# Kernel tuning notes

Measured on AMD Instinct MI355X. Metric: run time of the kernel, lower is better.

Reference implementation:

```python
import jax, jax.numpy as jnp
import numpy as np

N_N = 100000
N_E = 1600000
IN_DIM = 128
OUT_DIM = 128


def setup_inputs() -> dict:
    key = jax.random.key(0)
    k1, k2, k3, k4 = jax.random.split(key, 4)
    feats_n = jax.random.normal(k1, (N_N, IN_DIM), dtype=jnp.float32)
    # hs: guarantee every node appears at least once as a row (head) so degree > 0,
    # matching well-posed inputs for D**(-1/2) in the original module.
    hs = jnp.concatenate([
        jnp.arange(N_N, dtype=jnp.int64),
        jax.random.randint(k2, (N_E - N_N,), 0, N_N, dtype=jnp.int64),
    ])
    ts = jax.random.randint(k3, (N_E,), 0, N_N, dtype=jnp.int64)
    edges = jnp.stack([hs, ts], axis=0)  # [2, N_e]
    # Linear weight: normal(0,1) scaled by 1/sqrt(out_dim), no bias.
    weight = jax.random.normal(k4, (OUT_DIM, IN_DIM), dtype=jnp.float32) / np.sqrt(OUT_DIM)
    return {"feats_n": feats_n, "edges": edges, "weight": weight}


def reference(feats_n, edges, weight):
    hs, ts = edges[0], edges[1]
    n = feats_n.shape[0]
    # Degree = row-sum of adjacency (rows indexed by hs)
    deg = jax.ops.segment_sum(jnp.ones_like(hs, dtype=feats_n.dtype), hs, num_segments=n)
    sqrt_d_inv = deg ** (-0.5)  # [N_n]
    scaled = sqrt_d_inv[:, None] * feats_n  # [N_n, d]
    # SpMM: out[h] = sum over edges (h, t) of scaled[t]
    agg = jax.ops.segment_sum(scaled[ts], hs, num_segments=n)  # [N_n, d]
    msg = sqrt_d_inv[:, None] * agg
    out = msg @ weight.T  # Linear, no bias
    return jax.nn.relu(out)
```

## Files before the change

kernel.cpp:

```cpp
#include <hip/hip_runtime.h>

#define IN_DIM 128
#define CAP 64
#define NODE_SHIFT 8
#define BIN_NODES 256
#define NB_MAX 512
#define BCAP 5120
#define BINCAP_E 10240
#define CHUNK 4096
#define SMEM_BYTES 32768

typedef __attribute__((ext_vector_type(8))) short bf16x8;
typedef __attribute__((ext_vector_type(4))) float f32x4;
typedef __attribute__((ext_vector_type(2))) float f32x2;

struct PtLds { int hist[NB_MAX]; int base[NB_MAX]; unsigned int sp[CHUNK]; };
struct BsLds { unsigned int sp[BCAP]; int lcur[BIN_NODES]; int sbase[BIN_NODES];
               int wsum[4]; };

__device__ __forceinline__ unsigned short f2bf(float f) {
    unsigned int u = __float_as_uint(f);
    u += 0x7FFFu + ((u >> 16) & 1u);
    return (unsigned short)(u >> 16);
}

__device__ __forceinline__ void dev_partition(char* smem, int c, const int* __restrict__ edges,
                                              int n_e, int nbins,
                                              unsigned int* __restrict__ pairs,
                                              int* __restrict__ bincur) {
    PtLds* pt = (PtLds*)smem;
    int tid = threadIdx.x;
    int e0 = c * CHUNK;
    int nloc = n_e - e0;
    if (nloc > CHUNK) nloc = CHUNK;
    int nloc4 = nloc >> 2;
    const int* hsrc = edges + e0;
    const int* tsrc = edges + n_e + e0;
    for (int i = tid; i < nbins; i += 256) pt->hist[i] = 0;
    __syncthreads();
    for (int j = tid; j < nloc4; j += 256) {
        int4 hv = ((const int4*)hsrc)[j];
        int4 tv = ((const int4*)tsrc)[j];
        pt->sp[4 * j + 0] = ((unsigned int)(hv.x & 255) << 17) | (unsigned int)tv.x;
        pt->sp[4 * j + 1] = ((unsigned int)(hv.y & 255) << 17) | (unsigned int)tv.y;
        pt->sp[4 * j + 2] = ((unsigned int)(hv.z & 255) << 17) | (unsigned int)tv.z;
        pt->sp[4 * j + 3] = ((unsigned int)(hv.w & 255) << 17) | (unsigned int)tv.w;
        atomicAdd(&pt->hist[hv.x >> NODE_SHIFT], 1);
        atomicAdd(&pt->hist[hv.y >> NODE_SHIFT], 1);
        atomicAdd(&pt->hist[hv.z >> NODE_SHIFT], 1);
        atomicAdd(&pt->hist[hv.w >> NODE_SHIFT], 1);
    }
    for (int i = (nloc4 << 2) + tid; i < nloc; i += 256) {
        int h = hsrc[i];
        pt->sp[i] = ((unsigned int)(h & 255) << 17) | (unsigned int)tsrc[i];
        atomicAdd(&pt->hist[h >> NODE_SHIFT], 1);
    }
    __syncthreads();
    for (int b = tid; b < nbins; b += 256) {
        int cc = pt->hist[b];
        pt->base[b] = cc ? atomicAdd(&bincur[b], cc) : 0;
        pt->hist[b] = 0;
    }
    __syncthreads();
    for (int j = tid; j < nloc4; j += 256) {
        int4 hv = ((const int4*)hsrc)[j];
        int bi[4] = {hv.x >> NODE_SHIFT, hv.y >> NODE_SHIFT,
                     hv.z >> NODE_SHIFT, hv.w >> NODE_SHIFT};
        #pragma unroll
        for (int k = 0; k < 4; ++k) {
            int b = bi[k];
            int pos = atomicAdd(&pt->hist[b], 1);
            int g = pt->base[b] + pos;
            if (g < BCAP) pairs[(size_t)b * BCAP + g] = pt->sp[4 * j + k];
        }
    }
    for (int i = (nloc4 << 2) + tid; i < nloc; i += 256) {
        int b = hsrc[i] >> NODE_SHIFT;
        int pos = atomicAdd(&pt->hist[b], 1);
        int g = pt->base[b] + pos;
        if (g < BCAP) pairs[(size_t)b * BCAP + g] = pt->sp[i];
    }
    __syncthreads();
}

__device__ __forceinline__ void dev_binscatter(char* smem, int b,
                                               const unsigned int* __restrict__ pairs,
                                               const int* __restrict__ bincur,
                                               int* __restrict__ bucket,
                                               int2* __restrict__ rowinfo,
                                               float* __restrict__ rsd, int n_n) {
    BsLds* bs = (BsLds*)smem;
    int tid = threadIdx.x;
    bs->lcur[tid] = 0;
    __syncthreads();
    int n = bincur[b];
    if (n > BCAP) n = BCAP;
    const unsigned int* pp = pairs + (size_t)b * BCAP;
    for (int i = tid; i < n; i += 256) {
        unsigned int p = pp[i];
        bs->sp[i] = p;
        atomicAdd(&bs->lcur[p >> 17], 1);
    }
    __syncthreads();
    int draw = bs->lcur[tid];
    int dcap = draw < CAP ? draw : CAP;
    int v = (dcap + 15) & ~15;
    int lane = tid & 63, w = tid >> 6;
    int x = v;
    #pragma unroll
    for (int off = 1; off < 64; off <<= 1) {
        int y = __shfl_up(x, off);
        if (lane >= off) x += y;
    }
    if (lane == 63) bs->wsum[w] = x;
    __syncthreads();
    int wo = 0;
    for (int k = 0; k < w; ++k) wo += bs->wsum[k];
    int mybase = wo + x - v;
    bs->sbase[tid] = mybase;
    bs->lcur[tid] = 0;
    __syncthreads();
    int gbase = b * BINCAP_E;
    for (int i = tid; i < n; i += 256) {
        unsigned int p = bs->sp[i];
        int li = p >> 17;
        int t = p & 0x1FFFF;
        int pos = atomicAdd(&bs->lcur[li], 1);
        if (pos < CAP) {
            int idx = bs->sbase[li] + pos;
            if (idx < BINCAP_E) bucket[gbase + idx] = t;
        }
    }
    __syncthreads();
    int h = (b << NODE_SHIFT) + tid;
    if (h < n_n) {
        for (int s = dcap; s < v; ++s) {
            int idx = mybase + s;
            if (idx < BINCAP_E) bucket[gbase + idx] = n_n;
        }
        rowinfo[h] = make_int2(gbase + mybase, dcap);
        rsd[h] = draw > 0 ? rsqrtf((float)draw) : 0.0f;
    } else if (h == n_n) {
        rsd[n_n] = 0.0f;
    }
    __syncthreads();
}

__device__ __forceinline__ void dev_wconv(char* smem, const float* __restrict__ W) {
    bf16x8* wl = (bf16x8*)smem;
    int tid = threadIdx.x;
    #pragma unroll
    for (int k = 0; k < 8; ++k) {
        int gi = tid + k * 256;
        int n = gi >> 4, g = gi & 15;
        const float* wp = W + n * IN_DIM + g * 8;
        float4 a = *(const float4*)wp;
        float4 b2 = *(const float4*)(wp + 4);
        bf16x8 v;
        v[0] = (short)f2bf(a.x); v[1] = (short)f2bf(a.y);
        v[2] = (short)f2bf(a.z); v[3] = (short)f2bf(a.w);
        v[4] = (short)f2bf(b2.x); v[5] = (short)f2bf(b2.y);
        v[6] = (short)f2bf(b2.z); v[7] = (short)f2bf(b2.w);
        wl[n * 16 + (g ^ (n & 7))] = v;
    }
    __syncthreads();
}

__device__ __forceinline__ void dev_gemm(char* smem, int mb, const float* __restrict__ X,
                                         unsigned short* __restrict__ Y2, int M) {
    const bf16x8* wl = (const bf16x8*)smem;
    int tid = threadIdx.x;
    int slab = mb * 4 + (tid >> 6);
    int m0 = slab * 16;
    if (m0 >= M) return;
    int l = tid & 63;
    int lm = l & 15, lk = l >> 4;
    int row = m0 + lm;
    int rowc = row < M ? row : M - 1;
    bf16x8 xf[4];
    const float* xbase = X + (size_t)rowc * IN_DIM + lk * 8;
    #pragma unroll
    for (int ks = 0; ks < 4; ++ks) {
        float4 a = *(const float4*)(xbase + ks * 32);
        float4 b2 = *(const float4*)(xbase + ks * 32 + 4);
        bf16x8 v;
        v[0] = (short)f2bf(a.x); v[1] = (short)f2bf(a.y);
        v[2] = (short)f2bf(a.z); v[3] = (short)f2bf(a.w);
        v[4] = (short)f2bf(b2.x); v[5] = (short)f2bf(b2.y);
        v[6] = (short)f2bf(b2.z); v[7] = (short)f2bf(b2.w);
        xf[ks] = v;
    }
    #pragma unroll
    for (int nt = 0; nt < 8; ++nt) {
        f32x4 acc = {0.f, 0.f, 0.f, 0.f};
        #pragma unroll
        for (int ks = 0; ks < 4; ++ks) {
            int nn = nt * 16 + lm;
            int g = ks * 4 + lk;
            bf16x8 wf = wl[nn * 16 + (g ^ (nn & 7))];
            acc = __builtin_amdgcn_mfma_f32_16x16x32_bf16(wf, xf[ks], acc, 0, 0, 0);
        }
        if (row < M) {
            unsigned int lo = (unsigned int)f2bf(acc[0]) |
                              ((unsigned int)f2bf(acc[1]) << 16);
            unsigned int hi = (unsigned int)f2bf(acc[2]) |
                              ((unsigned int)f2bf(acc[3]) << 16);
            uint2* yp = (uint2*)(Y2 + (size_t)row * IN_DIM + nt * 16 + lk * 4);
            *yp = make_uint2(lo, hi);
        }
    }
}

__global__ __launch_bounds__(256, 4) void k_phaseA(const int* __restrict__ edges, int n_e,
                                                   int nbins, int npart, int mbA, int split,
                                                   unsigned int* __restrict__ pairs,
                                                   int* __restrict__ bincur,
                                                   const float* __restrict__ X,
                                                   const float* __restrict__ W,
                                                   unsigned short* __restrict__ Y2, int n_n) {
    extern __shared__ char smem[];
    int bid = blockIdx.x, NB = gridDim.x;
    if (bid < split) {
        for (int c = bid; c < npart; c += split)
            dev_partition(smem, c, edges, n_e, nbins, pairs, bincur);
    } else {
        dev_wconv(smem, W);
        for (int mb = bid - split; mb < mbA; mb += NB - split)
            dev_gemm(smem, mb, X, Y2, n_n);
    }
}

__global__ __launch_bounds__(256, 4) void k_phaseB(int nbins, int mbA, int nmf, int split,
                                                   const unsigned int* __restrict__ pairs,
                                                   const int* __restrict__ bincur,
                                                   int* __restrict__ bucket,
                                                   int2* __restrict__ rowinfo,
                                                   float* __restrict__ rsd,
                                                   const float* __restrict__ X,
                                                   const float* __restrict__ W,
                                                   unsigned short* __restrict__ Y2, int n_n) {
    extern __shared__ char smem[];
    int bid = blockIdx.x, NB = gridDim.x;
    if (bid < split) {
        for (int b = bid; b < nbins; b += split)
            dev_binscatter(smem, b, pairs, bincur, bucket, rowinfo, rsd, n_n);
    } else {
        dev_wconv(smem, W);
        for (int mb = mbA + (bid - split); mb < nmf; mb += NB - split)
            dev_gemm(smem, mb, X, Y2, n_n);
    }
}

__global__ __launch_bounds__(256) void k_agg(const uint4* __restrict__ Y4,
                                             const int* __restrict__ bucket,
                                             const int2* __restrict__ rowinfo,
                                             const float* __restrict__ rsd,
                                             float* __restrict__ out, int n_n) {
    int gw = (int)((blockIdx.x * 256u + threadIdx.x) >> 6);
    int lane = threadIdx.x & 63;
    if (gw >= n_n) return;
    int2 ri = rowinfo[gw];
    int d = ri.y;
    int nb = (d + 15) >> 4;
    const uint4* bk4 = (const uint4*)(bucket + ri.x);
    int grp = lane >> 4, a = lane & 15;
    f32x2 a0 = {0.f, 0.f}, a1 = {0.f, 0.f}, a2 = {0.f, 0.f}, a3 = {0.f, 0.f};

    uint4 tv = bk4[grp];
    for (int b = 0; b < nb; ++b) {
        int bn = (b + 1 < nb) ? b + 1 : b;
        uint4 tvn = bk4[bn * 4 + grp];
        float s0 = rsd[tv.x], s1 = rsd[tv.y], s2 = rsd[tv.z], s3 = rsd[tv.w];
        uint4 v0 = Y4[(size_t)tv.x * 16 + a];
        uint4 v1 = Y4[(size_t)tv.y * 16 + a];
        uint4 v2 = Y4[(size_t)tv.z * 16 + a];
        uint4 v3 = Y4[(size_t)tv.w * 16 + a];
        #define ACCUM(V, S)                                                   \
        {                                                                     \
            f32x2 sv; sv[0] = (S); sv[1] = (S);                               \
            f32x2 x;                                                          \
            x[0] = __uint_as_float((V).x << 16);                              \
            x[1] = __uint_as_float((V).x & 0xffff0000u);                      \
            asm("v_pk_fma_f32 %0, %1, %2, %0" : "+v"(a0) : "v"(x), "v"(sv));  \
            x[0] = __uint_as_float((V).y << 16);                              \
            x[1] = __uint_as_float((V).y & 0xffff0000u);                      \
            asm("v_pk_fma_f32 %0, %1, %2, %0" : "+v"(a1) : "v"(x), "v"(sv));  \
            x[0] = __uint_as_float((V).z << 16);                              \
            x[1] = __uint_as_float((V).z & 0xffff0000u);                      \
            asm("v_pk_fma_f32 %0, %1, %2, %0" : "+v"(a2) : "v"(x), "v"(sv));  \
            x[0] = __uint_as_float((V).w << 16);                              \
            x[1] = __uint_as_float((V).w & 0xffff0000u);                      \
            asm("v_pk_fma_f32 %0, %1, %2, %0" : "+v"(a3) : "v"(x), "v"(sv));  \
        }
        ACCUM(v0, s0) ACCUM(v1, s1) ACCUM(v2, s2) ACCUM(v3, s3)
        #undef ACCUM
        tv = tvn;
    }
    #define MERGE(A)                                                          \
    {                                                                         \
        A[0] += __shfl_xor(A[0], 16); A[1] += __shfl_xor(A[1], 16);           \
        A[0] += __shfl_xor(A[0], 32); A[1] += __shfl_xor(A[1], 32);           \
    }
    MERGE(a0) MERGE(a1) MERGE(a2) MERGE(a3)
    #undef MERGE
    if (lane < 16) {
        float s = rsd[gw];
        float4 o0 = make_float4(fmaxf(a0[0] * s, 0.f), fmaxf(a0[1] * s, 0.f),
                                fmaxf(a1[0] * s, 0.f), fmaxf(a1[1] * s, 0.f));
        float4 o1 = make_float4(fmaxf(a2[0] * s, 0.f), fmaxf(a2[1] * s, 0.f),
                                fmaxf(a3[0] * s, 0.f), fmaxf(a3[1] * s, 0.f));
        float4* op = (float4*)(out + (size_t)gw * IN_DIM + a * 8);
        op[0] = o0;
        op[1] = o1;
    }
}

extern "C" void kernel_launch(void* const* d_in, const int* in_sizes, int n_in,
                              void* d_out, int out_size, void* d_ws, size_t ws_size,
                              hipStream_t stream) {
    const float* X = (const float*)d_in[0];
    const int* edges = (const int*)d_in[1];
    const float* W = (const float*)d_in[2];
    int n_n = in_sizes[0] / IN_DIM;
    int n_e = in_sizes[1] / 2;
    int nbins = (n_n + BIN_NODES - 1) >> NODE_SHIFT;

    char* ws = (char*)d_ws;
    size_t o = 0;
    auto take = [&](size_t bytes) -> char* {
        char* p = ws + o;
        o += (bytes + 511) & ~(size_t)511;
        return p;
    };
    float* rsd = (float*)take((size_t)(n_n + 1) * 4);
    int2* rowinfo = (int2*)take((size_t)n_n * 8);
    int* bucket = (int*)take((size_t)nbins * BINCAP_E * 4);
    unsigned short* Y2 = (unsigned short*)take((size_t)(n_n + 1) * IN_DIM * 2);
    unsigned int* pairs = (unsigned int*)take((size_t)nbins * BCAP * 4);
    int* bincur = (int*)take((size_t)nbins * 4);

    int nslab = (n_n + 15) / 16;
    int nmf = (nslab + 3) / 4;
    int mbA = (nmf * 5) / 6;
    int npart = (n_e + CHUNK - 1) / CHUNK;
    int split = nbins;

    hipMemsetAsync(bincur, 0, (size_t)nbins * 4, stream);
    k_phaseA<<<1024, 256, SMEM_BYTES, stream>>>(edges, n_e, nbins, npart, mbA, split,
                                                pairs, bincur, X, W, Y2, n_n);
    k_phaseB<<<1024, 256, SMEM_BYTES, stream>>>(nbins, mbA, nmf, split, pairs, bincur,
                                                bucket, rowinfo, rsd, X, W, Y2, n_n);
    k_agg<<<(n_n + 3) / 4, 256, 0, stream>>>((const uint4*)Y2, bucket, rowinfo, rsd,
                                             (float*)d_out, n_n);
}
```

Baseline: 120.1 us.

## Quantize projected features to int8 with per-row scale for gather aggregation

The GEMM epilogue now quantizes each projected row to biased uint8 with a per-row absmax scale instead of storing bf16. The aggregation kernel gathers 8-byte instead of 16-byte chunks per lane, converts bytes with v_cvt_f32_ubyte, and folds the row scale into the edge coefficient. It removes the +128 bias afterwards using an accumulated sum of coefficients. This halves the random-gather traffic in the dominant SpMM stage, at the cost of int8 quantization error and an extra per-edge rowscale load.

```diff
diff --git a/kernel.cpp b/kernel.cpp
--- a/kernel.cpp
+++ b/kernel.cpp
@@ -88,7 +88,8 @@
                                                const int* __restrict__ bincur,
                                                int* __restrict__ bucket,
                                                int2* __restrict__ rowinfo,
-                                               float* __restrict__ rsd, int n_n) {
+                                               float* __restrict__ rsd,
+                                               float* __restrict__ rowscale, int n_n) {
     BsLds* bs = (BsLds*)smem;
     int tid = threadIdx.x;
     bs->lcur[tid] = 0;
@@ -142,6 +143,7 @@
         rsd[h] = draw > 0 ? rsqrtf((float)draw) : 0.0f;
     } else if (h == n_n) {
         rsd[n_n] = 0.0f;
+        rowscale[n_n] = 0.0f;
     }
     __syncthreads();
 }
@@ -167,7 +169,8 @@
 }
 
 __device__ __forceinline__ void dev_gemm(char* smem, int mb, const float* __restrict__ X,
-                                         unsigned short* __restrict__ Y2, int M) {
+                                         unsigned char* __restrict__ Y8,
+                                         float* __restrict__ rowscale, int M) {
     const bf16x8* wl = (const bf16x8*)smem;
     int tid = threadIdx.x;
     int slab = mb * 4 + (tid >> 6);
@@ -190,24 +193,40 @@
         v[6] = (short)f2bf(b2.z); v[7] = (short)f2bf(b2.w);
         xf[ks] = v;
     }
+    f32x4 acc[8];
     #pragma unroll
     for (int nt = 0; nt < 8; ++nt) {
-        f32x4 acc = {0.f, 0.f, 0.f, 0.f};
+        acc[nt][0] = 0.f; acc[nt][1] = 0.f; acc[nt][2] = 0.f; acc[nt][3] = 0.f;
         #pragma unroll
         for (int ks = 0; ks < 4; ++ks) {
             int nn = nt * 16 + lm;
             int g = ks * 4 + lk;
             bf16x8 wf = wl[nn * 16 + (g ^ (nn & 7))];
-            acc = __builtin_amdgcn_mfma_f32_16x16x32_bf16(wf, xf[ks], acc, 0, 0, 0);
-        }
-        if (row < M) {
-            unsigned int lo = (unsigned int)f2bf(acc[0]) |
-                              ((unsigned int)f2bf(acc[1]) << 16);
-            unsigned int hi = (unsigned int)f2bf(acc[2]) |
-                              ((unsigned int)f2bf(acc[3]) << 16);
-            uint2* yp = (uint2*)(Y2 + (size_t)row * IN_DIM + nt * 16 + lk * 4);
-            *yp = make_uint2(lo, hi);
-        }
+            acc[nt] = __builtin_amdgcn_mfma_f32_16x16x32_bf16(wf, xf[ks], acc[nt], 0, 0, 0);
+        }
+    }
+    float mx = 0.f;
+    #pragma unroll
+    for (int nt = 0; nt < 8; ++nt) {
+        mx = fmaxf(mx, fmaxf(fmaxf(fabsf(acc[nt][0]), fabsf(acc[nt][1])),
+                             fmaxf(fabsf(acc[nt][2]), fabsf(acc[nt][3]))));
+    }
+    mx = fmaxf(mx, __shfl_xor(mx, 16));
+    mx = fmaxf(mx, __shfl_xor(mx, 32));
+    float inv = mx > 0.f ? 127.0f / mx : 0.f;
+    if (row >= M) return;
+    if (lk == 0) rowscale[row] = mx * (1.0f / 127.0f);
+    unsigned char* yb = Y8 + (size_t)row * IN_DIM;
+    #pragma unroll
+    for (int nt = 0; nt < 8; ++nt) {
+        unsigned int wd = 0;
+        #pragma unroll
+        for (int r = 0; r < 4; ++r) {
+            int q = (int)rintf(acc[nt][r] * inv);
+            q = q < -127 ? -127 : (q > 127 ? 127 : q);
+            wd |= (unsigned int)(q + 128) << (8 * r);
+        }
+        *(unsigned int*)(yb + nt * 16 + lk * 4) = wd;
     }
 }
 
@@ -217,7 +236,8 @@
                                                    int* __restrict__ bincur,
                                                    const float* __restrict__ X,
                                                    const float* __restrict__ W,
-                                                   unsigned short* __restrict__ Y2, int n_n) {
+                                                   unsigned char* __restrict__ Y8,
+                                                   float* __restrict__ rowscale, int n_n) {
     extern __shared__ char smem[];
     int bid = blockIdx.x, NB = gridDim.x;
     if (bid < split) {
@@ -226,7 +246,7 @@
     } else {
         dev_wconv(smem, W);
         for (int mb = bid - split; mb < mbA; mb += NB - split)
-            dev_gemm(smem, mb, X, Y2, n_n);
+            dev_gemm(smem, mb, X, Y8, rowscale, n_n);
     }
 }
 
@@ -238,23 +258,25 @@
                                                    float* __restrict__ rsd,
                                                    const float* __restrict__ X,
                                                    const float* __restrict__ W,
-                                                   unsigned short* __restrict__ Y2, int n_n) {
+                                                   unsigned char* __restrict__ Y8,
+                                                   float* __restrict__ rowscale, int n_n) {
     extern __shared__ char smem[];
     int bid = blockIdx.x, NB = gridDim.x;
     if (bid < split) {
         for (int b = bid; b < nbins; b += split)
-            dev_binscatter(smem, b, pairs, bincur, bucket, rowinfo, rsd, n_n);
+            dev_binscatter(smem, b, pairs, bincur, bucket, rowinfo, rsd, rowscale, n_n);
     } else {
         dev_wconv(smem, W);
         for (int mb = mbA + (bid - split); mb < nmf; mb += NB - split)
-            dev_gemm(smem, mb, X, Y2, n_n);
-    }
-}
-
-__global__ __launch_bounds__(256) void k_agg(const uint4* __restrict__ Y4,
+            dev_gemm(smem, mb, X, Y8, rowscale, n_n);
+    }
+}
+
+__global__ __launch_bounds__(256) void k_agg(const uint2* __restrict__ Y8v,
                                              const int* __restrict__ bucket,
                                              const int2* __restrict__ rowinfo,
                                              const float* __restrict__ rsd,
+                                             const float* __restrict__ rowscale,
                                              float* __restrict__ out, int n_n) {
     int gw = (int)((blockIdx.x * 256u + threadIdx.x) >> 6);
     int lane = threadIdx.x & 63;
@@ -265,34 +287,40 @@
     const uint4* bk4 = (const uint4*)(bucket + ri.x);
     int grp = lane >> 4, a = lane & 15;
     f32x2 a0 = {0.f, 0.f}, a1 = {0.f, 0.f}, a2 = {0.f, 0.f}, a3 = {0.f, 0.f};
+    float S = 0.f;
+
+    #define CVT0(U, F) asm("v_cvt_f32_ubyte0 %0, %1" : "=v"(F) : "v"(U));
+    #define CVT1(U, F) asm("v_cvt_f32_ubyte1 %0, %1" : "=v"(F) : "v"(U));
+    #define CVT2(U, F) asm("v_cvt_f32_ubyte2 %0, %1" : "=v"(F) : "v"(U));
+    #define CVT3(U, F) asm("v_cvt_f32_ubyte3 %0, %1" : "=v"(F) : "v"(U));
 
     uint4 tv = bk4[grp];
     for (int b = 0; b < nb; ++b) {
         int bn = (b + 1 < nb) ? b + 1 : b;
         uint4 tvn = bk4[bn * 4 + grp];
-        float s0 = rsd[tv.x], s1 = rsd[tv.y], s2 = rsd[tv.z], s3 = rsd[tv.w];
-        uint4 v0 = Y4[(size_t)tv.x * 16 + a];
-        uint4 v1 = Y4[(size_t)tv.y * 16 + a];
-        uint4 v2 = Y4[(size_t)tv.z * 16 + a];
-        uint4 v3 = Y4[(size_t)tv.w * 16 + a];
-        #define ACCUM(V, S)                                                   \
+        float c0 = rsd[tv.x] * rowscale[tv.x];
+        float c1 = rsd[tv.y] * rowscale[tv.y];
+        float c2 = rsd[tv.z] * rowscale[tv.z];
+        float c3 = rsd[tv.w] * rowscale[tv.w];
+        uint2 v0 = Y8v[(size_t)tv.x * 16 + a];
+        uint2 v1 = Y8v[(size_t)tv.y * 16 + a];
+        uint2 v2 = Y8v[(size_t)tv.z * 16 + a];
+        uint2 v3 = Y8v[(size_t)tv.w * 16 + a];
+        #define ACCUM(V, C)                                                   \
         {                                                                     \
-            f32x2 sv; sv[0] = (S); sv[1] = (S);                               \
+            S += (C);                                                         \
+            f32x2 sv; sv[0] = (C); sv[1] = (C);                               \
             f32x2 x;                                                          \
-            x[0] = __uint_as_float((V).x << 16);                              \
-            x[1] = __uint_as_float((V).x & 0xffff0000u);                      \
+            CVT0((V).x, x[0]) CVT1((V).x, x[1])                               \
             asm("v_pk_fma_f32 %0, %1, %2, %0" : "+v"(a0) : "v"(x), "v"(sv));  \
-            x[0] = __uint_as_float((V).y << 16);                              \
-            x[1] = __uint_as_float((V).y & 0xffff0000u);                      \
+            CVT2((V).x, x[0]) CVT3((V).x, x[1])                               \
             asm("v_pk_fma_f32 %0, %1, %2, %0" : "+v"(a1) : "v"(x), "v"(sv));  \
-            x[0] = __uint_as_float((V).z << 16);                              \
-            x[1] = __uint_as_float((V).z & 0xffff0000u);                      \
+            CVT0((V).y, x[0]) CVT1((V).y, x[1])                               \
             asm("v_pk_fma_f32 %0, %1, %2, %0" : "+v"(a2) : "v"(x), "v"(sv));  \
-            x[0] = __uint_as_float((V).w << 16);                              \
-            x[1] = __uint_as_float((V).w & 0xffff0000u);                      \
+            CVT2((V).y, x[0]) CVT3((V).y, x[1])                               \
             asm("v_pk_fma_f32 %0, %1, %2, %0" : "+v"(a3) : "v"(x), "v"(sv));  \
         }
-        ACCUM(v0, s0) ACCUM(v1, s1) ACCUM(v2, s2) ACCUM(v3, s3)
+        ACCUM(v0, c0) ACCUM(v1, c1) ACCUM(v2, c2) ACCUM(v3, c3)
         #undef ACCUM
         tv = tvn;
     }
@@ -303,16 +331,23 @@
     }
     MERGE(a0) MERGE(a1) MERGE(a2) MERGE(a3)
     #undef MERGE
+    S += __shfl_xor(S, 16);
+    S += __shfl_xor(S, 32);
     if (lane < 16) {
+        float adj = 128.0f * S;
         float s = rsd[gw];
-        float4 o0 = make_float4(fmaxf(a0[0] * s, 0.f), fmaxf(a0[1] * s, 0.f),
-                                fmaxf(a1[0] * s, 0.f), fmaxf(a1[1] * s, 0.f));
-        float4 o1 = make_float4(fmaxf(a2[0] * s, 0.f), fmaxf(a2[1] * s, 0.f),
-                                fmaxf(a3[0] * s, 0.f), fmaxf(a3[1] * s, 0.f));
+        float4 o0 = make_float4(fmaxf((a0[0] - adj) * s, 0.f), fmaxf((a0[1] - adj) * s, 0.f),
+                                fmaxf((a1[0] - adj) * s, 0.f), fmaxf((a1[1] - adj) * s, 0.f));
+        float4 o1 = make_float4(fmaxf((a2[0] - adj) * s, 0.f), fmaxf((a2[1] - adj) * s, 0.f),
+                                fmaxf((a3[0] - adj) * s, 0.f), fmaxf((a3[1] - adj) * s, 0.f));
         float4* op = (float4*)(out + (size_t)gw * IN_DIM + a * 8);
         op[0] = o0;
         op[1] = o1;
     }
+    #undef CVT0
+    #undef CVT1
+    #undef CVT2
+    #undef CVT3
 }
 
 extern "C" void kernel_launch(void* const* d_in, const int* in_sizes, int n_in,
@@ -333,9 +368,10 @@
         return p;
     };
     float* rsd = (float*)take((size_t)(n_n + 1) * 4);
+    float* rowscale = (float*)take((size_t)(n_n + 1) * 4);
     int2* rowinfo = (int2*)take((size_t)n_n * 8);
     int* bucket = (int*)take((size_t)nbins * BINCAP_E * 4);
-    unsigned short* Y2 = (unsigned short*)take((size_t)(n_n + 1) * IN_DIM * 2);
+    unsigned char* Y8 = (unsigned char*)take((size_t)(n_n + 1) * IN_DIM);
     unsigned int* pairs = (unsigned int*)take((size_t)nbins * BCAP * 4);
     int* bincur = (int*)take((size_t)nbins * 4);
 
@@ -347,9 +383,9 @@
 
     hipMemsetAsync(bincur, 0, (size_t)nbins * 4, stream);
     k_phaseA<<<1024, 256, SMEM_BYTES, stream>>>(edges, n_e, nbins, npart, mbA, split,
-                                                pairs, bincur, X, W, Y2, n_n);
+                                                pairs, bincur, X, W, Y8, rowscale, n_n);
     k_phaseB<<<1024, 256, SMEM_BYTES, stream>>>(nbins, mbA, nmf, split, pairs, bincur,
-                                                bucket, rowinfo, rsd, X, W, Y2, n_n);
-    k_agg<<<(n_n + 3) / 4, 256, 0, stream>>>((const uint4*)Y2, bucket, rowinfo, rsd,
-                                             (float*)d_out, n_n);
-}
+                                                bucket, rowinfo, rsd, X, W, Y8, rowscale, n_n);
+    k_agg<<<(n_n + 3) / 4, 256, 0, stream>>>((const uint2*)Y8, bucket, rowinfo, rsd,
+                                             rowscale, (float*)d_out, n_n);
+}
```

After: 110.4 us. -8.0%, faster.
